# Kernel tuning notes

Hardware: AMD Instinct MI355X
Metric: run time of the kernel (lower is better)

Reference implementation:

```python
import jax, jax.numpy as jnp
import numpy as np

K = 3        # kernel_size
S = 2        # stride
SHIFT = 4    # shift_size
NEG = 0.2    # LeakyReLU slope


def conv2d(x, w, b, stride=1, pad=1):
    y = jax.lax.conv_general_dilated(x, w, (stride, stride), [(pad, pad), (pad, pad)],
                                     dimension_numbers=('NCHW', 'OIHW', 'NCHW'))
    return y + b[None, :, None, None]


def lrelu(x):
    return jnp.where(x >= 0, x, NEG * x)


def spatial_shift(x, s):
    # 4-direction grouped spatial shift (zero fill); Shift source not in snippet,
    # implemented S2-MLP style: channel groups shifted right/left/down/up by s.
    g = x.shape[1] // 4
    x1 = jnp.pad(x[:, :g, :, :-s], ((0, 0), (0, 0), (0, 0), (s, 0)))
    x2 = jnp.pad(x[:, g:2 * g, :, s:], ((0, 0), (0, 0), (0, 0), (0, s)))
    x3 = jnp.pad(x[:, 2 * g:3 * g, :-s, :], ((0, 0), (0, 0), (s, 0), (0, 0)))
    x4 = jnp.pad(x[:, 3 * g:, s:, :], ((0, 0), (0, 0), (0, s), (0, 0)))
    return jnp.concatenate([x1, x2, x3, x4], axis=1)


def setup_inputs() -> dict:
    key = jax.random.key(0)
    ks = jax.random.split(key, 8)
    B, C, T, H, W = 2, 64, 8, 128, 128
    sc = 0.05
    return {
        'x': jax.random.normal(ks[0], (B, C, T, H, W), jnp.float32),
        'w1': jax.random.normal(ks[1], (C, C, 3, 3), jnp.float32) * sc,
        'b1': jnp.zeros((C,), jnp.float32),
        'w2': jax.random.normal(ks[2], (C, C, 3, 3), jnp.float32) * sc,
        'b2': jnp.zeros((C,), jnp.float32),
        'wk1': jax.random.normal(ks[3], (C, C), jnp.float32) * sc,   # 1x1x1 conv3d
        'bk1': jnp.zeros((C,), jnp.float32),
        'wk2': jax.random.normal(ks[4], (C, C, 3, 3), jnp.float32) * sc,  # (1,3,3) conv3d
        'bk2': jnp.zeros((C,), jnp.float32),
        'wk3': jax.random.normal(ks[5], (K * K, C, 3, 3), jnp.float32) * sc,  # (1,3,3) strided
        'bk3': jnp.zeros((K * K,), jnp.float32),
    }


def reference(x, w1, b1, w2, b2, wk1, bk1, wk2, bk2, wk3, bk3):
    B, C, T, H, W = x.shape
    # ---- Xvo_shift, frames folded into batch ----
    xf = jnp.transpose(x, (0, 2, 1, 3, 4)).reshape(B * T, C, H, W)
    res = lrelu(conv2d(xf, w1, b1))
    res = spatial_shift(res, SHIFT) * res
    res = conv2d(res, w2, b2)
    xf = xf + res
    x5 = jnp.transpose(xf.reshape(B, T, C, H, W), (0, 2, 1, 3, 4))  # b c t h w
    # ---- kernel prediction (conv3d with temporal kernel 1 == per-frame conv2d) ----
    k = jnp.einsum('oc,bcthw->bothw', wk1, x5) + bk1[None, :, None, None, None]
    kf = jnp.transpose(k, (0, 2, 1, 3, 4)).reshape(B * T, C, H, W)
    kf = lrelu(conv2d(kf, wk2, bk2))
    kf = conv2d(kf, wk3, bk3, stride=S, pad=1)  # (B*T, K*K, Ho, Wo)
    Ho, Wo = kf.shape[-2], kf.shape[-1]
    kernel = jnp.transpose(kf.reshape(B, T, K * K, Ho, Wo), (0, 3, 4, 1, 2))
    kernel = kernel.reshape(B, Ho, Wo, T * K * K)
    kernel = jax.nn.softmax(kernel, axis=-1)
    kernel = kernel.reshape(B, 1, Ho, Wo, T, K, K)
    # ---- unfold with replicate padding, then weighted reduce ----
    num_pad = (K - S + 1) // 2
    xp = jnp.pad(x5, ((0, 0), (0, 0), (0, 0), (num_pad, num_pad), (num_pad, num_pad)), mode='edge')
    patches = jnp.stack([
        jnp.stack([xp[:, :, :, i:i + S * Ho:S, j:j + S * Wo:S] for j in range(K)], axis=-1)
        for i in range(K)], axis=-2)  # (B,C,T,Ho,Wo,K,K)
    patches = jnp.transpose(patches, (0, 1, 3, 4, 2, 5, 6))  # (B,C,Ho,Wo,T,K,K)
    out = jnp.sum(patches * kernel, axis=(-3, -2, -1))  # (B,C,Ho,Wo)
    return out
```

## Files before the change

kernel.cpp:

```cpp
#include <hip/hip_runtime.h>
#include <hip/hip_bf16.h>
#include <math.h>

#define Wd 128
#define Hd 128
#define HW 16384
#define CH 64
#define TT 8
#define NEGS 0.2f
#define PW 130
#define ROWB (PW * CH * 2)

typedef unsigned short u16;
typedef u16 u16x8 __attribute__((ext_vector_type(8)));
typedef u16 u16x4 __attribute__((ext_vector_type(4)));
typedef short bf16x8 __attribute__((ext_vector_type(8)));
typedef float f32x4 __attribute__((ext_vector_type(4)));

__device__ __forceinline__ u16 tobf(float v) {
  __hip_bfloat16 h = __float2bfloat16(v);
  return __builtin_bit_cast(u16, h);
}
__device__ __forceinline__ float bf2f(u16 u) {
  unsigned x = ((unsigned)u) << 16;
  return __builtin_bit_cast(float, x);
}
__device__ __forceinline__ void gload_lds16(const void* g, void* l) {
  __builtin_amdgcn_global_load_lds(
      (const __attribute__((address_space(1))) unsigned int*)g,
      (__attribute__((address_space(3))) unsigned int*)l, 16, 0, 0);
}

__global__ __launch_bounds__(256) void prep_k(
    const float* __restrict__ w1, const float* __restrict__ w2,
    const float* __restrict__ wk2, const float* __restrict__ wk1,
    const float* __restrict__ wk3,
    short* __restrict__ Wp1, short* __restrict__ Wp2,
    short* __restrict__ Wp4, short* __restrict__ Wk1b,
    short* __restrict__ Wp3)
{
  const int bx = blockIdx.x, y = blockIdx.y;
  if (bx < 144) {
    const float* w = (y == 0) ? w1 : (y == 1) ? w2 : wk2;
    short* out = (y == 0) ? Wp1 : (y == 1) ? Wp2 : Wp4;
    int i = bx * 256 + threadIdx.x;
    int cout = i / 576, k = i - cout * 576;
    int off = k >> 6, cin = k & 63;
    int dy = off / 3, dx = off - dy * 3;
    int gi = cout * 72 + (k >> 3);
    int go = ((gi ^ (cout & 7)) << 3) + (k & 7);
    out[go] = (short)tobf(w[((cout * 64 + cin) * 3 + dy) * 3 + dx]);
  } else if (y == 0 && bx < 160) {
    int i = (bx - 144) * 256 + threadIdx.x;
    Wk1b[i] = (short)tobf(wk1[i]);
  } else if (y == 1) {
    int i = (bx - 144) * 256 + threadIdx.x;
    if (i < 9216) {
      int cout = i / 576, k = i - cout * 576;
      int off = k >> 6, cin = k & 63;
      int dy = off / 3, dx = off - dy * 3;
      float v = (cout < 9) ? wk3[((cout * 64 + cin) * 3 + dy) * 3 + dx] : 0.f;
      Wp3[i] = (short)tobf(v);
    }
  }
}

__global__ __launch_bounds__(256) void xprep_k(const float* __restrict__ x,
                                               u16* __restrict__ outb)
{
  __shared__ __align__(16) u16 Sw[128 * 72];
  const int f = blockIdx.x, b = f >> 3, t = f & 7;
  const int ph = blockIdx.y;
  const int h = ph - 1;
  const bool rowok = (h >= 0 && h < Hd);
  const int tid = threadIdx.x;

  if (rowok) {
    const int cl = tid >> 5;
    const int m  = tid & 31;
#pragma unroll 1
    for (int cc = 0; cc < 8; ++cc) {
      const int c = cc * 8 + cl;
      const float* src = x + (((size_t)(b * 64 + c) * 8 + t) * HW) + (size_t)h * Wd;
      const int oct = c >> 3, e = c & 7;
#pragma unroll
      for (int j = 0; j < 4; ++j) {
        const int w = m + 32 * j;
        const float v = src[w];
        const int s = oct ^ ((w + 1) & 7);
        Sw[w * 72 + s * 8 + e] = tobf(v);
      }
    }
  }
  __syncthreads();

  const size_t obase = ((size_t)f * PW + ph) * PW * CH;
#pragma unroll 1
  for (int g = tid; g < 1040; g += 256) {
    const int ppw = g >> 3, u = g & 7;
    u16x8 pk = (u16x8)0;
    if (rowok && ppw >= 1 && ppw <= 128)
      pk = *(const u16x8*)(Sw + (ppw - 1) * 72 + u * 8);
    *(u16x8*)(outb + obase + (size_t)ppw * CH + u * 8) = pk;
  }
}

__global__ __launch_bounds__(256) void padzero_k(u16* __restrict__ a,
                                                 u16* __restrict__ b)
{
  u16* buf = (blockIdx.z == 0) ? a : b;
  const int f = blockIdx.y;
  u16* fb = buf + (size_t)f * PW * PW * CH;
  const int g = blockIdx.x * 256 + threadIdx.x;
  if (g >= 4128) return;
  size_t off;
  if (g < 1040)      off = (size_t)g * 8;
  else if (g < 2080) off = (size_t)129 * PW * CH + (size_t)(g - 1040) * 8;
  else if (g < 3104) { int r = (g - 2080) >> 3, u = (g - 2080) & 7;
                       off = ((size_t)(r + 1) * PW + 0) * CH + u * 8; }
  else               { int r = (g - 3104) >> 3, u = (g - 3104) & 7;
                       off = ((size_t)(r + 1) * PW + 129) * CH + u * 8; }
  *(u16x8*)(fb + off) = (u16x8)0;
}

__global__ __launch_bounds__(256) void shmul_k(const u16* __restrict__ r1,
                                               u16* __restrict__ sm)
{
  const int f = blockIdx.x;
  const int ph = blockIdx.y;
  const int us = threadIdx.x & 7;
  const int p0 = threadIdx.x >> 3;
#pragma unroll
  for (int i = 0; i < 5; ++i) {
    const int ppw = p0 + 32 * i;
    if (ppw < PW) {
      const int ub = us ^ (ppw & 7);
      const int g = ub >> 1;
      const int dw = (g == 0) ? -4 : (g == 1) ? 4 : 0;
      const int dh = (g == 2) ? -4 : (g == 3) ? 4 : 0;
      const size_t idx = ((size_t)f * PW + ph) * PW * CH + (size_t)ppw * CH;
      u16x8 v = *(const u16x8*)(r1 + idx + us * 8);
      const int h2 = ph + dh, w2 = ppw + dw;
      const bool okp = (h2 >= 1 && h2 <= Hd && w2 >= 1 && w2 <= Wd);
      const int h2c = min(max(h2, 0), PW - 1);
      const int w2c = min(max(w2, 0), PW - 1);
      const int u2 = (dw != 0) ? (us ^ 4) : us;
      u16x8 pv = *(const u16x8*)(r1 + ((size_t)f * PW + h2c) * PW * CH +
                                 (size_t)w2c * CH + u2 * 8);
      u16x8 o;
#pragma unroll
      for (int j = 0; j < 8; ++j) {
        float pr = okp ? bf2f(v[j]) * bf2f(pv[j]) : 0.f;
        o[j] = tobf(pr);
      }
      *(u16x8*)(sm + idx + us * 8) = o;
    }
  }
}

__global__ __launch_bounds__(512) void conv3x3_pers_k(
    const u16* __restrict__ inp, const short* __restrict__ wsw,
    const float* __restrict__ bias, u16* __restrict__ outb)
{
  extern __shared__ __align__(16) char smem[];
  short* Ws = (short*)smem;
  u16* Xb0 = (u16*)(smem + 73728);
  u16* Xb1 = (u16*)(smem + 73728 + 44032);

  const int bid = blockIdx.x;
  const int f = bid >> 4, hy = bid & 15;
  const int h0 = hy * 8;
  const int tid = threadIdx.x;
  const int lane = tid & 63;
  const int wv = __builtin_amdgcn_readfirstlane(tid >> 6);
  const int l15 = lane & 15;
  const int oct = lane >> 4;

  f32x4 b4[4];
#pragma unroll
  for (int cg = 0; cg < 4; ++cg)
#pragma unroll
    for (int rr = 0; rr < 4; ++rr)
      b4[cg][rr] = bias[cg * 16 + oct * 4 + rr];

  {
    const char* gs = (const char*)wsw;
    char* ld = (char*)Ws;
#pragma unroll 1
    for (int i = wv; i < 72; i += 8)
      gload_lds16(gs + i * 1024 + lane * 16, ld + i * 1024);
  }

  const char* fbp = (const char*)(inp + (size_t)f * PW * PW * CH);

  {
    const char* tb = fbp + (size_t)h0 * ROWB;
    char* ld = (char*)Xb0;
#pragma unroll 1
    for (int i = wv; i < 43; i += 8) {
      const int ob = i * 1024 + lane * 16;
      const int row = ob / 4352;
      const int rem = ob - row * 4352;
      gload_lds16(tb + (size_t)row * ROWB + rem, ld + i * 1024);
    }
  }

#pragma unroll 1
  for (int it = 0; it < 4; ++it) {
    __syncthreads();
    u16* Xc = (it & 1) ? Xb1 : Xb0;
    u16* Xn = (it & 1) ? Xb0 : Xb1;
    if (it < 3) {
      const char* tb = fbp + (size_t)h0 * ROWB + (size_t)(it + 1) * 32 * CH * 2;
      char* ld = (char*)Xn;
#pragma unroll 1
      for (int i = wv; i < 43; i += 8) {
        const int ob = i * 1024 + lane * 16;
        const int row = ob / 4352;
        const int rem = ob - row * 4352;
        gload_lds16(tb + (size_t)row * ROWB + rem, ld + i * 1024);
      }
    }
    const int w0 = it * 32;

    f32x4 acc[4][2];
#pragma unroll
    for (int i = 0; i < 4; ++i)
#pragma unroll
      for (int j = 0; j < 2; ++j) acc[i][j] = (f32x4)0.f;

#pragma unroll 1
    for (int s = 0; s < 18; ++s) {
      const int o = s >> 1;
      const int dy = o / 3, dx = o - dy * 3;
      const int half = s & 1;
      bf16x8 a[4];
#pragma unroll
      for (int cg = 0; cg < 4; ++cg) {
        const int gi = (cg * 16 + l15) * 72 + s * 4 + oct;
        a[cg] = *(const bf16x8*)(Ws + ((gi ^ (l15 & 7)) << 3));
      }
#pragma unroll
      for (int pt = 0; pt < 2; ++pt) {
        const int r = wv + dy;
        const int cc = pt * 16 + dx + l15;
        const int p = r * 34 + cc;
        const int co = ((half * 4 + oct) ^ (cc & 7)) << 3;
        bf16x8 b = *(const bf16x8*)((const short*)Xc + p * 64 + co);
#pragma unroll
        for (int cg = 0; cg < 4; ++cg)
          acc[cg][pt] = __builtin_amdgcn_mfma_f32_16x16x32_bf16(a[cg], b, acc[cg][pt], 0, 0, 0);
      }
    }

#pragma unroll
    for (int cg = 0; cg < 4; ++cg)
#pragma unroll
      for (int pt = 0; pt < 2; ++pt) {
        const int py = h0 + wv;
        const int px = w0 + pt * 16 + l15;
        const int pph = py + 1, ppw = px + 1;
        const int unit = (cg * 2 + (oct >> 1)) ^ (ppw & 7);
        u16x4 pk;
#pragma unroll
        for (int rr = 0; rr < 4; ++rr) {
          float t2 = acc[cg][pt][rr] + b4[cg][rr];
          t2 = (t2 >= 0.f) ? t2 : NEGS * t2;
          pk[rr] = tobf(t2);
        }
        *(u16x4*)(outb + ((size_t)f * PW + pph) * PW * CH + (size_t)ppw * CH +
                  unit * 8 + (oct & 1) * 4) = pk;
      }
  }
}

__global__ __launch_bounds__(512) void convx5_pers_k(
    const u16* __restrict__ inp, const short* __restrict__ wsw,
    const float* __restrict__ bias, const u16* __restrict__ xp,
    const short* __restrict__ w1b, const float* __restrict__ b1x1,
    u16* __restrict__ outx, u16* __restrict__ outk)
{
  extern __shared__ __align__(16) char smem[];
  short* Ws = (short*)smem;
  u16* Xb0 = (u16*)(smem + 73728);
  u16* Xb1 = (u16*)(smem + 73728 + 44032);

  const int bid = blockIdx.x;
  const int f = bid >> 4, hy = bid & 15;
  const int h0 = hy * 8;
  const int tid = threadIdx.x;
  const int lane = tid & 63;
  const int wv = __builtin_amdgcn_readfirstlane(tid >> 6);
  const int l15 = lane & 15;
  const int oct = lane >> 4;

  f32x4 b4[4], bb1[4];
#pragma unroll
  for (int cg = 0; cg < 4; ++cg)
#pragma unroll
    for (int rr = 0; rr < 4; ++rr) {
      b4[cg][rr]  = bias[cg * 16 + oct * 4 + rr];
      bb1[cg][rr] = b1x1[cg * 16 + oct * 4 + rr];
    }
  bf16x8 a1_0[4], a1_1[4];
#pragma unroll
  for (int cg = 0; cg < 4; ++cg) {
    a1_0[cg] = *(const bf16x8*)(w1b + (cg * 16 + l15) * 64 + 0 * 32 + oct * 8);
    a1_1[cg] = *(const bf16x8*)(w1b + (cg * 16 + l15) * 64 + 1 * 32 + oct * 8);
  }

  {
    const char* gs = (const char*)wsw;
    char* ld = (char*)Ws;
#pragma unroll 1
    for (int i = wv; i < 72; i += 8)
      gload_lds16(gs + i * 1024 + lane * 16, ld + i * 1024);
  }

  const size_t fbase = (size_t)f * PW * PW * CH;
  const char* fbp = (const char*)(inp + fbase);

  {
    const char* tb = fbp + (size_t)h0 * ROWB;
    char* ld = (char*)Xb0;
#pragma unroll 1
    for (int i = wv; i < 43; i += 8) {
      const int ob = i * 1024 + lane * 16;
      const int row = ob / 4352;
      const int rem = ob - row * 4352;
      gload_lds16(tb + (size_t)row * ROWB + rem, ld + i * 1024);
    }
  }

#pragma unroll 1
  for (int it = 0; it < 4; ++it) {
    __syncthreads();
    u16* Xc = (it & 1) ? Xb1 : Xb0;
    u16* Xn = (it & 1) ? Xb0 : Xb1;
    if (it < 3) {
      const char* tb = fbp + (size_t)h0 * ROWB + (size_t)(it + 1) * 32 * CH * 2;
      char* ld = (char*)Xn;
#pragma unroll 1
      for (int i = wv; i < 43; i += 8) {
        const int ob = i * 1024 + lane * 16;
        const int row = ob / 4352;
        const int rem = ob - row * 4352;
        gload_lds16(tb + (size_t)row * ROWB + rem, ld + i * 1024);
      }
    }
    const int w0 = it * 32;
    const int pph = h0 + wv + 1;

    u16x4 xrv[4][2];
    size_t gaddr[4][2];
#pragma unroll
    for (int cg = 0; cg < 4; ++cg)
#pragma unroll
      for (int pt = 0; pt < 2; ++pt) {
        const int lc = pt * 16 + l15;
        const int ppw = w0 + lc + 1;
        const int unitg = (cg * 2 + (oct >> 1)) ^ (ppw & 7);
        gaddr[cg][pt] = fbase + ((size_t)pph * PW + ppw) * CH + unitg * 8 + (oct & 1) * 4;
        xrv[cg][pt] = *(const u16x4*)(xp + gaddr[cg][pt]);
      }

    f32x4 acc[4][2];
#pragma unroll
    for (int i = 0; i < 4; ++i)
#pragma unroll
      for (int j = 0; j < 2; ++j) acc[i][j] = (f32x4)0.f;

#pragma unroll 1
    for (int s = 0; s < 18; ++s) {
      const int o = s >> 1;
      const int dy = o / 3, dx = o - dy * 3;
      const int half = s & 1;
      bf16x8 a[4];
#pragma unroll
      for (int cg = 0; cg < 4; ++cg) {
        const int gi = (cg * 16 + l15) * 72 + s * 4 + oct;
        a[cg] = *(const bf16x8*)(Ws + ((gi ^ (l15 & 7)) << 3));
      }
#pragma unroll
      for (int pt = 0; pt < 2; ++pt) {
        const int r = wv + dy;
        const int cc = pt * 16 + dx + l15;
        const int p = r * 34 + cc;
        const int co = ((half * 4 + oct) ^ (cc & 7)) << 3;
        bf16x8 b = *(const bf16x8*)((const short*)Xc + p * 64 + co);
#pragma unroll
        for (int cg = 0; cg < 4; ++cg)
          acc[cg][pt] = __builtin_amdgcn_mfma_f32_16x16x32_bf16(a[cg], b, acc[cg][pt], 0, 0, 0);
      }
    }

    __syncthreads();
    u16* Ys = Xc;

#pragma unroll
    for (int cg = 0; cg < 4; ++cg)
#pragma unroll
      for (int pt = 0; pt < 2; ++pt) {
        const int lc = pt * 16 + l15;
        const int p2 = wv * 32 + lc;
        u16x4 pk;
#pragma unroll
        for (int rr = 0; rr < 4; ++rr) {
          float v = acc[cg][pt][rr] + b4[cg][rr] + bf2f(xrv[cg][pt][rr]);
          pk[rr] = tobf(v);
        }
        *(u16x4*)(outx + gaddr[cg][pt]) = pk;
        const int unit2 = (cg * 2 + (oct >> 1)) ^ (p2 & 7);
        *(u16x4*)(Ys + p2 * 64 + unit2 * 8 + (oct & 1) * 4) = pk;
      }
    __syncthreads();

    f32x4 acc2[4][2];
#pragma unroll
    for (int i = 0; i < 4; ++i)
#pragma unroll
      for (int j = 0; j < 2; ++j) acc2[i][j] = (f32x4)0.f;

#pragma unroll
    for (int pt = 0; pt < 2; ++pt) {
      const int p2 = wv * 32 + pt * 16 + l15;
      const int co0 = ((0 * 4 + oct) ^ (p2 & 7)) << 3;
      const int co1 = ((1 * 4 + oct) ^ (p2 & 7)) << 3;
      bf16x8 bv0 = *(const bf16x8*)((const short*)Ys + p2 * 64 + co0);
      bf16x8 bv1 = *(const bf16x8*)((const short*)Ys + p2 * 64 + co1);
#pragma unroll
      for (int cg = 0; cg < 4; ++cg) {
        acc2[cg][pt] = __builtin_amdgcn_mfma_f32_16x16x32_bf16(a1_0[cg], bv0, acc2[cg][pt], 0, 0, 0);
        acc2[cg][pt] = __builtin_amdgcn_mfma_f32_16x16x32_bf16(a1_1[cg], bv1, acc2[cg][pt], 0, 0, 0);
      }
    }

#pragma unroll
    for (int cg = 0; cg < 4; ++cg)
#pragma unroll
      for (int pt = 0; pt < 2; ++pt) {
        const int lc = pt * 16 + l15;
        const int ppw = w0 + lc + 1;
        const int unit = (cg * 2 + (oct >> 1)) ^ (ppw & 7);
        u16x4 pk;
#pragma unroll
        for (int rr = 0; rr < 4; ++rr)
          pk[rr] = tobf(acc2[cg][pt][rr] + bb1[cg][rr]);
        *(u16x4*)(outk + fbase + ((size_t)pph * PW + ppw) * CH +
                  unit * 8 + (oct & 1) * 4) = pk;
      }
  }
}

__global__ __launch_bounds__(512) void convs2m_k(
    const u16* __restrict__ inb, const short* __restrict__ w3b,
    const float* __restrict__ bk3, float* __restrict__ sc)
{
  extern __shared__ __align__(16) char smem[];
  u16* St = (u16*)smem;
  const int hy = blockIdx.x;
  const int f  = blockIdx.y;
  const int tid = threadIdx.x;
  const int lane = tid & 63;
  const int wv = __builtin_amdgcn_readfirstlane(tid >> 6);
  const int l15 = lane & 15;
  const int oct = lane >> 4;

  const char* fbp = (const char*)(inb + (size_t)f * PW * PW * CH) +
                    (size_t)(8 * hy) * ROWB;
  char* ld = (char*)St;
#pragma unroll 1
  for (int g = tid; g < 9360; g += 512)
    gload_lds16(fbp + g * 16, ld + g * 16);
  __syncthreads();

  f32x4 acc[2];
  acc[0] = (f32x4)0.f;
  acc[1] = (f32x4)0.f;

#pragma unroll 2
  for (int s = 0; s < 18; ++s) {
    const int o = s >> 1;
    const int dy = o / 3, dx = o - dy * 3;
    const int half = s & 1;
    bf16x8 a = *(const bf16x8*)(w3b + l15 * 576 + s * 32 + oct * 8);
#pragma unroll
    for (int pg = 0; pg < 2; ++pg) {
      const int g = wv * 2 + pg;
      const int ho_l = g >> 2, wg = g & 3;
      const int wo = wg * 16 + l15;
      const int irow = 2 * ho_l + dy;
      const int ipx = 2 * wo + dx;
      const int slot = (half * 4 + oct) ^ (ipx & 7);
      bf16x8 b = *(const bf16x8*)((const short*)St + (irow * PW + ipx) * 64 + slot * 8);
      acc[pg] = __builtin_amdgcn_mfma_f32_16x16x32_bf16(a, b, acc[pg], 0, 0, 0);
    }
  }

#pragma unroll
  for (int pg = 0; pg < 2; ++pg) {
    const int g = wv * 2 + pg;
    const int ho = hy * 4 + (g >> 2);
    const int wo = (g & 3) * 16 + l15;
#pragma unroll
    for (int rr = 0; rr < 4; ++rr) {
      const int kk = oct * 4 + rr;
      if (kk < 9)
        sc[((size_t)f * 9 + kk) * 4096 + ho * 64 + wo] = acc[pg][rr] + bk3[kk];
    }
  }
}

__global__ __launch_bounds__(256) void gather2_k(
    const u16* __restrict__ x5p, const float* __restrict__ sc,
    float* __restrict__ out)
{
  const int hx = blockIdx.x;
  const int ho = blockIdx.y;
  const int b  = blockIdx.z;
  const int wo0 = hx * 32;
  __shared__ float wl[32 * 73];
  for (int e = threadIdx.x; e < 32 * 72; e += 256) {
    const int wo = e & 31, k = e >> 5;
    const int t = k / 9, kk = k - t * 9;
    wl[wo * 73 + k] = sc[((size_t)((b * 8 + t) * 9 + kk)) * 4096 + ho * 64 + wo0 + wo];
  }
  __syncthreads();
  if (threadIdx.x < 32) {
    float* row = &wl[threadIdx.x * 73];
    float mx = -1e30f;
#pragma unroll
    for (int i = 0; i < 72; ++i) mx = fmaxf(mx, row[i]);
    float sum = 0.f;
#pragma unroll
    for (int i = 0; i < 72; ++i) { float e2 = __expf(row[i] - mx); row[i] = e2; sum += e2; }
    const float inv = 1.f / sum;
#pragma unroll
    for (int i = 0; i < 72; ++i) row[i] *= inv;
  }
  __syncthreads();
  const int lane = threadIdx.x & 63;
  const int wv = threadIdx.x >> 6;
  const int u = lane & 7;
  const int wol = (lane >> 3) + wv * 8;
  const int wo = wo0 + wol;
  float acc[8];
#pragma unroll
  for (int j = 0; j < 8; ++j) acc[j] = 0.f;
#pragma unroll 1
  for (int t = 0; t < 8; ++t) {
    const int f = b * 8 + t;
    const size_t fb = (size_t)f * PW * PW * CH;
    const float* wrow = &wl[wol * 73 + t * 9];
#pragma unroll
    for (int di = 0; di < 3; ++di) {
      const int pph = min(max(2 * ho + di, 1), 128);
#pragma unroll
      for (int dj = 0; dj < 3; ++dj) {
        const int ppw = min(max(2 * wo + dj, 1), 128);
        const int unit = u ^ (ppw & 7);
        u16x8 pk = *(const u16x8*)(x5p + fb + ((size_t)pph * PW + ppw) * CH + unit * 8);
        const float wq = wrow[di * 3 + dj];
#pragma unroll
        for (int j = 0; j < 8; ++j)
          acc[j] = fmaf(bf2f(pk[j]), wq, acc[j]);
      }
    }
  }
  const int obase = ((b * 64 + u * 8) * 64 + ho) * 64 + wo;
#pragma unroll
  for (int j = 0; j < 8; ++j)
    out[obase + j * 4096] = acc[j];
}

extern "C" void kernel_launch(void* const* d_in, const int* in_sizes, int n_in,
                              void* d_out, int out_size, void* d_ws, size_t ws_size,
                              hipStream_t stream)
{
  const float* x   = (const float*)d_in[0];
  const float* w1  = (const float*)d_in[1];
  const float* b1  = (const float*)d_in[2];
  const float* w2  = (const float*)d_in[3];
  const float* b2  = (const float*)d_in[4];
  const float* wk1 = (const float*)d_in[5];
  const float* bk1 = (const float*)d_in[6];
  const float* wk2 = (const float*)d_in[7];
  const float* bk2 = (const float*)d_in[8];
  const float* wk3 = (const float*)d_in[9];
  const float* bk3 = (const float*)d_in[10];
  float* outp = (float*)d_out;

  const size_t PADB = (size_t)16 * PW * PW * CH * 2;
  char* ws = (char*)d_ws;
  u16*  P1      = (u16*)ws;
  u16*  P2      = (u16*)(ws + PADB);
  u16*  P3      = (u16*)(ws + 2 * PADB);
  u16*  P4      = (u16*)(ws + 3 * PADB);
  u16*  P5      = (u16*)(ws + 4 * PADB);
  float* scores = (float*)(ws + 5 * PADB);
  short* Wp1    = (short*)(ws + 5 * PADB + 2359296);
  short* Wp2    = Wp1 + 36864;
  short* Wp4    = Wp2 + 36864;
  short* Wk1b   = Wp4 + 36864;
  short* Wp3    = Wk1b + 4096;
  (void)ws_size; (void)in_sizes; (void)n_in; (void)out_size;

  hipFuncSetAttribute((const void*)conv3x3_pers_k,
                      hipFuncAttributeMaxDynamicSharedMemorySize, 161792);
  hipFuncSetAttribute((const void*)convx5_pers_k,
                      hipFuncAttributeMaxDynamicSharedMemorySize, 161792);
  hipFuncSetAttribute((const void*)convs2m_k,
                      hipFuncAttributeMaxDynamicSharedMemorySize, 149760);

  prep_k<<<dim3(180, 3), 256, 0, stream>>>(w1, w2, wk2, wk1, wk3,
                                           Wp1, Wp2, Wp4, Wk1b, Wp3);
  xprep_k<<<dim3(16, PW), 256, 0, stream>>>(x, P1);
  padzero_k<<<dim3(17, 16, 2), 256, 0, stream>>>(P2, P3);

  conv3x3_pers_k<<<dim3(256), 512, 161792, stream>>>(P1, Wp1, b1, P2);
  shmul_k<<<dim3(16, PW), 256, 0, stream>>>(P2, P5);
  convx5_pers_k<<<dim3(256), 512, 161792, stream>>>(P5, Wp2, b2, P1, Wk1b, bk1, P4, P3);
  conv3x3_pers_k<<<dim3(256), 512, 161792, stream>>>(P3, Wp4, bk2, P1);
  convs2m_k<<<dim3(16, 16), 512, 149760, stream>>>(P1, Wp3, bk3, scores);
  gather2_k<<<dim3(2, 64, 2), 256, 0, stream>>>(P4, scores, outp);
}
```

Before: 156.7 us.

## Halve conv row tiles, split output channels across waves, read weights from global

The three 3x3 conv kernels now cover 4 rows per block instead of 8, and each wave owns one row plus half of the output channels, so the grid doubles to 512 blocks. Weights are no longer staged in LDS. They are re-laid out in prep_k so each wave can read them directly from global memory (cached), which cuts LDS per block from about 158KB to 51KB. This allows several blocks per CU and raises occupancy. The cost is more global and L2 weight traffic and a larger halo overhead for each input tile.

```diff
diff --git a/kernel.cpp b/kernel.cpp
--- a/kernel.cpp
+++ b/kernel.cpp
@@ -47,8 +47,7 @@
     int cout = i / 576, k = i - cout * 576;
     int off = k >> 6, cin = k & 63;
     int dy = off / 3, dx = off - dy * 3;
-    int gi = cout * 72 + (k >> 3);
-    int go = ((gi ^ (cout & 7)) << 3) + (k & 7);
+    int go = ((k >> 5) * 64 + cout) * 32 + (k & 31);
     out[go] = (short)tobf(w[((cout * 64 + cin) * 3 + dy) * 3 + dx]);
   } else if (y == 0 && bx < 160) {
     int i = (bx - 144) * 256 + threadIdx.x;
@@ -158,50 +157,46 @@
   }
 }
 
-__global__ __launch_bounds__(512) void conv3x3_pers_k(
-    const u16* __restrict__ inp, const short* __restrict__ wsw,
+__global__ __launch_bounds__(512) void conv3x3_pers2_k(
+    const u16* __restrict__ inp, const short* __restrict__ wgt,
     const float* __restrict__ bias, u16* __restrict__ outb)
 {
   extern __shared__ __align__(16) char smem[];
-  short* Ws = (short*)smem;
-  u16* Xb0 = (u16*)(smem + 73728);
-  u16* Xb1 = (u16*)(smem + 73728 + 44032);
+  u16* Xb0 = (u16*)smem;
+  u16* Xb1 = (u16*)(smem + 26112);
 
   const int bid = blockIdx.x;
-  const int f = bid >> 4, hy = bid & 15;
-  const int h0 = hy * 8;
+  const int f = bid >> 5, hy = bid & 31;
+  const int h0 = hy * 4;
   const int tid = threadIdx.x;
   const int lane = tid & 63;
   const int wv = __builtin_amdgcn_readfirstlane(tid >> 6);
+  const int r0 = wv >> 1;
+  const int chh = wv & 1;
   const int l15 = lane & 15;
   const int oct = lane >> 4;
 
-  f32x4 b4[4];
-#pragma unroll
-  for (int cg = 0; cg < 4; ++cg)
+  f32x4 b4[2];
+#pragma unroll
+  for (int cg = 0; cg < 2; ++cg)
 #pragma unroll
     for (int rr = 0; rr < 4; ++rr)
-      b4[cg][rr] = bias[cg * 16 + oct * 4 + rr];
-
-  {
-    const char* gs = (const char*)wsw;
-    char* ld = (char*)Ws;
-#pragma unroll 1
-    for (int i = wv; i < 72; i += 8)
-      gload_lds16(gs + i * 1024 + lane * 16, ld + i * 1024);
-  }
-
-  const char* fbp = (const char*)(inp + (size_t)f * PW * PW * CH);
+      b4[cg][rr] = bias[chh * 32 + cg * 16 + oct * 4 + rr];
+
+  const size_t fbase = (size_t)f * PW * PW * CH;
+  const char* fbp = (const char*)(inp + fbase);
 
   {
     const char* tb = fbp + (size_t)h0 * ROWB;
     char* ld = (char*)Xb0;
 #pragma unroll 1
-    for (int i = wv; i < 43; i += 8) {
+    for (int i = wv; i < 26; i += 8) {
       const int ob = i * 1024 + lane * 16;
-      const int row = ob / 4352;
-      const int rem = ob - row * 4352;
-      gload_lds16(tb + (size_t)row * ROWB + rem, ld + i * 1024);
+      if (ob < 26112) {
+        const int row = ob / 4352;
+        const int rem = ob - row * 4352;
+        gload_lds16(tb + (size_t)row * ROWB + rem, ld + ob);
+      }
     }
   }
 
@@ -214,18 +209,20 @@
       const char* tb = fbp + (size_t)h0 * ROWB + (size_t)(it + 1) * 32 * CH * 2;
       char* ld = (char*)Xn;
 #pragma unroll 1
-      for (int i = wv; i < 43; i += 8) {
+      for (int i = wv; i < 26; i += 8) {
         const int ob = i * 1024 + lane * 16;
-        const int row = ob / 4352;
-        const int rem = ob - row * 4352;
-        gload_lds16(tb + (size_t)row * ROWB + rem, ld + i * 1024);
+        if (ob < 26112) {
+          const int row = ob / 4352;
+          const int rem = ob - row * 4352;
+          gload_lds16(tb + (size_t)row * ROWB + rem, ld + ob);
+        }
       }
     }
     const int w0 = it * 32;
 
-    f32x4 acc[4][2];
-#pragma unroll
-    for (int i = 0; i < 4; ++i)
+    f32x4 acc[2][2];
+#pragma unroll
+    for (int i = 0; i < 2; ++i)
 #pragma unroll
       for (int j = 0; j < 2; ++j) acc[i][j] = (f32x4)0.f;
 
@@ -234,33 +231,30 @@
       const int o = s >> 1;
       const int dy = o / 3, dx = o - dy * 3;
       const int half = s & 1;
-      bf16x8 a[4];
-#pragma unroll
-      for (int cg = 0; cg < 4; ++cg) {
-        const int gi = (cg * 16 + l15) * 72 + s * 4 + oct;
-        a[cg] = *(const bf16x8*)(Ws + ((gi ^ (l15 & 7)) << 3));
-      }
+      bf16x8 a[2];
+#pragma unroll
+      for (int cg = 0; cg < 2; ++cg)
+        a[cg] = *(const bf16x8*)(wgt + (s * 64 + chh * 32 + cg * 16 + l15) * 32 + oct * 8);
 #pragma unroll
       for (int pt = 0; pt < 2; ++pt) {
-        const int r = wv + dy;
+        const int r = r0 + dy;
         const int cc = pt * 16 + dx + l15;
         const int p = r * 34 + cc;
         const int co = ((half * 4 + oct) ^ (cc & 7)) << 3;
         bf16x8 b = *(const bf16x8*)((const short*)Xc + p * 64 + co);
 #pragma unroll
-        for (int cg = 0; cg < 4; ++cg)
+        for (int cg = 0; cg < 2; ++cg)
           acc[cg][pt] = __builtin_amdgcn_mfma_f32_16x16x32_bf16(a[cg], b, acc[cg][pt], 0, 0, 0);
       }
     }
 
 #pragma unroll
-    for (int cg = 0; cg < 4; ++cg)
+    for (int cg = 0; cg < 2; ++cg)
 #pragma unroll
       for (int pt = 0; pt < 2; ++pt) {
-        const int py = h0 + wv;
-        const int px = w0 + pt * 16 + l15;
-        const int pph = py + 1, ppw = px + 1;
-        const int unit = (cg * 2 + (oct >> 1)) ^ (ppw & 7);
+        const int pph = h0 + r0 + 1;
+        const int ppw = w0 + pt * 16 + l15 + 1;
+        const int unit = (chh * 4 + cg * 2 + (oct >> 1)) ^ (ppw & 7);
         u16x4 pk;
 #pragma unroll
         for (int rr = 0; rr < 4; ++rr) {
@@ -268,53 +262,47 @@
           t2 = (t2 >= 0.f) ? t2 : NEGS * t2;
           pk[rr] = tobf(t2);
         }
-        *(u16x4*)(outb + ((size_t)f * PW + pph) * PW * CH + (size_t)ppw * CH +
+        *(u16x4*)(outb + fbase + ((size_t)pph * PW + ppw) * CH +
                   unit * 8 + (oct & 1) * 4) = pk;
       }
   }
 }
 
-__global__ __launch_bounds__(512) void convx5_pers_k(
-    const u16* __restrict__ inp, const short* __restrict__ wsw,
+__global__ __launch_bounds__(512) void convx5_pers2_k(
+    const u16* __restrict__ inp, const short* __restrict__ wgt,
     const float* __restrict__ bias, const u16* __restrict__ xp,
     const short* __restrict__ w1b, const float* __restrict__ b1x1,
     u16* __restrict__ outx, u16* __restrict__ outk)
 {
   extern __shared__ __align__(16) char smem[];
-  short* Ws = (short*)smem;
-  u16* Xb0 = (u16*)(smem + 73728);
-  u16* Xb1 = (u16*)(smem + 73728 + 44032);
+  u16* Xb0 = (u16*)smem;
+  u16* Xb1 = (u16*)(smem + 26112);
 
   const int bid = blockIdx.x;
-  const int f = bid >> 4, hy = bid & 15;
-  const int h0 = hy * 8;
+  const int f = bid >> 5, hy = bid & 31;
+  const int h0 = hy * 4;
   const int tid = threadIdx.x;
   const int lane = tid & 63;
   const int wv = __builtin_amdgcn_readfirstlane(tid >> 6);
+  const int r0 = wv >> 1;
+  const int chh = wv & 1;
   const int l15 = lane & 15;
   const int oct = lane >> 4;
 
-  f32x4 b4[4], bb1[4];
-#pragma unroll
-  for (int cg = 0; cg < 4; ++cg)
+  f32x4 b4[2], bb1[2];
+#pragma unroll
+  for (int cg = 0; cg < 2; ++cg)
 #pragma unroll
     for (int rr = 0; rr < 4; ++rr) {
-      b4[cg][rr]  = bias[cg * 16 + oct * 4 + rr];
-      bb1[cg][rr] = b1x1[cg * 16 + oct * 4 + rr];
-    }
-  bf16x8 a1_0[4], a1_1[4];
-#pragma unroll
-  for (int cg = 0; cg < 4; ++cg) {
-    a1_0[cg] = *(const bf16x8*)(w1b + (cg * 16 + l15) * 64 + 0 * 32 + oct * 8);
-    a1_1[cg] = *(const bf16x8*)(w1b + (cg * 16 + l15) * 64 + 1 * 32 + oct * 8);
-  }
-
-  {
-    const char* gs = (const char*)wsw;
-    char* ld = (char*)Ws;
-#pragma unroll 1
-    for (int i = wv; i < 72; i += 8)
-      gload_lds16(gs + i * 1024 + lane * 16, ld + i * 1024);
+      b4[cg][rr]  = bias[chh * 32 + cg * 16 + oct * 4 + rr];
+      bb1[cg][rr] = b1x1[chh * 32 + cg * 16 + oct * 4 + rr];
+    }
+  bf16x8 a1_0[2], a1_1[2];
+#pragma unroll
+  for (int cg = 0; cg < 2; ++cg) {
+    const int kout = chh * 32 + cg * 16 + l15;
+    a1_0[cg] = *(const bf16x8*)(w1b + kout * 64 + 0 * 32 + oct * 8);
+    a1_1[cg] = *(const bf16x8*)(w1b + kout * 64 + 1 * 32 + oct * 8);
   }
 
   const size_t fbase = (size_t)f * PW * PW * CH;
@@ -324,11 +312,13 @@
     const char* tb = fbp + (size_t)h0 * ROWB;
     char* ld = (char*)Xb0;
 #pragma unroll 1
-    for (int i = wv; i < 43; i += 8) {
+    for (int i = wv; i < 26; i += 8) {
       const int ob = i * 1024 + lane * 16;
-      const int row = ob / 4352;
-      const int rem = ob - row * 4352;
-      gload_lds16(tb + (size_t)row * ROWB + rem, ld + i * 1024);
+      if (ob < 26112) {
+        const int row = ob / 4352;
+        const int rem = ob - row * 4352;
+        gload_lds16(tb + (size_t)row * ROWB + rem, ld + ob);
+      }
     }
   }
 
@@ -341,32 +331,33 @@
       const char* tb = fbp + (size_t)h0 * ROWB + (size_t)(it + 1) * 32 * CH * 2;
       char* ld = (char*)Xn;
 #pragma unroll 1
-      for (int i = wv; i < 43; i += 8) {
+      for (int i = wv; i < 26; i += 8) {
         const int ob = i * 1024 + lane * 16;
-        const int row = ob / 4352;
-        const int rem = ob - row * 4352;
-        gload_lds16(tb + (size_t)row * ROWB + rem, ld + i * 1024);
+        if (ob < 26112) {
+          const int row = ob / 4352;
+          const int rem = ob - row * 4352;
+          gload_lds16(tb + (size_t)row * ROWB + rem, ld + ob);
+        }
       }
     }
     const int w0 = it * 32;
-    const int pph = h0 + wv + 1;
-
-    u16x4 xrv[4][2];
-    size_t gaddr[4][2];
-#pragma unroll
-    for (int cg = 0; cg < 4; ++cg)
+    const int pph = h0 + r0 + 1;
+
+    u16x4 xrv[2][2];
+    size_t gaddr[2][2];
+#pragma unroll
+    for (int cg = 0; cg < 2; ++cg)
 #pragma unroll
       for (int pt = 0; pt < 2; ++pt) {
-        const int lc = pt * 16 + l15;
-        const int ppw = w0 + lc + 1;
-        const int unitg = (cg * 2 + (oct >> 1)) ^ (ppw & 7);
+        const int ppw = w0 + pt * 16 + l15 + 1;
+        const int unitg = (chh * 4 + cg * 2 + (oct >> 1)) ^ (ppw & 7);
         gaddr[cg][pt] = fbase + ((size_t)pph * PW + ppw) * CH + unitg * 8 + (oct & 1) * 4;
         xrv[cg][pt] = *(const u16x4*)(xp + gaddr[cg][pt]);
       }
 
-    f32x4 acc[4][2];
-#pragma unroll
-    for (int i = 0; i < 4; ++i)
+    f32x4 acc[2][2];
+#pragma unroll
+    for (int i = 0; i < 2; ++i)
 #pragma unroll
       for (int j = 0; j < 2; ++j) acc[i][j] = (f32x4)0.f;
 
@@ -375,21 +366,19 @@
       const int o = s >> 1;
       const int dy = o / 3, dx = o - dy * 3;
       const int half = s & 1;
-      bf16x8 a[4];
-#pragma unroll
-      for (int cg = 0; cg < 4; ++cg) {
-        const int gi = (cg * 16 + l15) * 72 + s * 4 + oct;
-        a[cg] = *(const bf16x8*)(Ws + ((gi ^ (l15 & 7)) << 3));
-      }
+      bf16x8 a[2];
+#pragma unroll
+      for (int cg = 0; cg < 2; ++cg)
+        a[cg] = *(const bf16x8*)(wgt + (s * 64 + chh * 32 + cg * 16 + l15) * 32 + oct * 8);
 #pragma unroll
       for (int pt = 0; pt < 2; ++pt) {
-        const int r = wv + dy;
+        const int r = r0 + dy;
         const int cc = pt * 16 + dx + l15;
         const int p = r * 34 + cc;
         const int co = ((half * 4 + oct) ^ (cc & 7)) << 3;
         bf16x8 b = *(const bf16x8*)((const short*)Xc + p * 64 + co);
 #pragma unroll
-        for (int cg = 0; cg < 4; ++cg)
+        for (int cg = 0; cg < 2; ++cg)
           acc[cg][pt] = __builtin_amdgcn_mfma_f32_16x16x32_bf16(a[cg], b, acc[cg][pt], 0, 0, 0);
       }
     }
@@ -398,11 +387,11 @@
     u16* Ys = Xc;
 
 #pragma unroll
-    for (int cg = 0; cg < 4; ++cg)
+    for (int cg = 0; cg < 2; ++cg)
 #pragma unroll
       for (int pt = 0; pt < 2; ++pt) {
         const int lc = pt * 16 + l15;
-        const int p2 = wv * 32 + lc;
+        const int p2 = r0 * 32 + lc;
         u16x4 pk;
 #pragma unroll
         for (int rr = 0; rr < 4; ++rr) {
@@ -410,44 +399,40 @@
           pk[rr] = tobf(v);
         }
         *(u16x4*)(outx + gaddr[cg][pt]) = pk;
-        const int unit2 = (cg * 2 + (oct >> 1)) ^ (p2 & 7);
+        const int unit2 = (chh * 4 + cg * 2 + (oct >> 1)) ^ (p2 & 7);
         *(u16x4*)(Ys + p2 * 64 + unit2 * 8 + (oct & 1) * 4) = pk;
       }
     __syncthreads();
 
-    f32x4 acc2[4][2];
-#pragma unroll
-    for (int i = 0; i < 4; ++i)
+    f32x4 acc2[2][2];
+#pragma unroll
+    for (int i = 0; i < 2; ++i)
 #pragma unroll
       for (int j = 0; j < 2; ++j) acc2[i][j] = (f32x4)0.f;
 
 #pragma unroll
     for (int pt = 0; pt < 2; ++pt) {
-      const int p2 = wv * 32 + pt * 16 + l15;
+      const int p2 = r0 * 32 + pt * 16 + l15;
       const int co0 = ((0 * 4 + oct) ^ (p2 & 7)) << 3;
       const int co1 = ((1 * 4 + oct) ^ (p2 & 7)) << 3;
       bf16x8 bv0 = *(const bf16x8*)((const short*)Ys + p2 * 64 + co0);
       bf16x8 bv1 = *(const bf16x8*)((const short*)Ys + p2 * 64 + co1);
 #pragma unroll
-      for (int cg = 0; cg < 4; ++cg) {
+      for (int cg = 0; cg < 2; ++cg) {
         acc2[cg][pt] = __builtin_amdgcn_mfma_f32_16x16x32_bf16(a1_0[cg], bv0, acc2[cg][pt], 0, 0, 0);
         acc2[cg][pt] = __builtin_amdgcn_mfma_f32_16x16x32_bf16(a1_1[cg], bv1, acc2[cg][pt], 0, 0, 0);
       }
     }
 
 #pragma unroll
-    for (int cg = 0; cg < 4; ++cg)
+    for (int cg = 0; cg < 2; ++cg)
 #pragma unroll
       for (int pt = 0; pt < 2; ++pt) {
-        const int lc = pt * 16 + l15;
-        const int ppw = w0 + lc + 1;
-        const int unit = (cg * 2 + (oct >> 1)) ^ (ppw & 7);
         u16x4 pk;
 #pragma unroll
         for (int rr = 0; rr < 4; ++rr)
           pk[rr] = tobf(acc2[cg][pt][rr] + bb1[cg][rr]);
-        *(u16x4*)(outk + fbase + ((size_t)pph * PW + ppw) * CH +
-                  unit * 8 + (oct & 1) * 4) = pk;
+        *(u16x4*)(outk + gaddr[cg][pt]) = pk;
       }
   }
 }
@@ -605,10 +590,10 @@
   short* Wp3    = Wk1b + 4096;
   (void)ws_size; (void)in_sizes; (void)n_in; (void)out_size;
 
-  hipFuncSetAttribute((const void*)conv3x3_pers_k,
-                      hipFuncAttributeMaxDynamicSharedMemorySize, 161792);
-  hipFuncSetAttribute((const void*)convx5_pers_k,
-                      hipFuncAttributeMaxDynamicSharedMemorySize, 161792);
+  hipFuncSetAttribute((const void*)conv3x3_pers2_k,
+                      hipFuncAttributeMaxDynamicSharedMemorySize, 52224);
+  hipFuncSetAttribute((const void*)convx5_pers2_k,
+                      hipFuncAttributeMaxDynamicSharedMemorySize, 52224);
   hipFuncSetAttribute((const void*)convs2m_k,
                       hipFuncAttributeMaxDynamicSharedMemorySize, 149760);
 
@@ -617,10 +602,10 @@
   xprep_k<<<dim3(16, PW), 256, 0, stream>>>(x, P1);
   padzero_k<<<dim3(17, 16, 2), 256, 0, stream>>>(P2, P3);
 
-  conv3x3_pers_k<<<dim3(256), 512, 161792, stream>>>(P1, Wp1, b1, P2);
+  conv3x3_pers2_k<<<dim3(512), 512, 52224, stream>>>(P1, Wp1, b1, P2);
   shmul_k<<<dim3(16, PW), 256, 0, stream>>>(P2, P5);
-  convx5_pers_k<<<dim3(256), 512, 161792, stream>>>(P5, Wp2, b2, P1, Wk1b, bk1, P4, P3);
-  conv3x3_pers_k<<<dim3(256), 512, 161792, stream>>>(P3, Wp4, bk2, P1);
+  convx5_pers2_k<<<dim3(512), 512, 52224, stream>>>(P5, Wp2, b2, P1, Wk1b, bk1, P4, P3);
+  conv3x3_pers2_k<<<dim3(512), 512, 52224, stream>>>(P3, Wp4, bk2, P1);
   convs2m_k<<<dim3(16, 16), 512, 149760, stream>>>(P1, Wp3, bk3, scores);
   gather2_k<<<dim3(2, 64, 2), 256, 0, stream>>>(P4, scores, outp);
 }
```

Result: slower. 209.4 us (+33.6%).
